# Performance work log

Hardware: AMD Instinct MI355X
Metric: run time of the kernel (lower is better)

The kernel has to match this reference:

```python
import jax, jax.numpy as jnp
import numpy as np

BITS = 4
GROUPSIZE = 128
IN_FEATURES = 4096
OUT_FEATURES = 11008
N_GROUPS = IN_FEATURES // GROUPSIZE  # 32
MASK = (1 << BITS) - 1  # 15


def setup_inputs() -> dict:
    key = jax.random.key(0)
    ks = jax.random.split(key, 5)
    x = jax.random.normal(ks[0], (2, 2048, IN_FEATURES), dtype=jnp.float32)
    qweight = jax.random.randint(ks[1], (IN_FEATURES // 8, OUT_FEATURES), 0, 2**31 - 1, dtype=jnp.int32)
    qzeros = jax.random.randint(ks[2], (N_GROUPS, OUT_FEATURES // 8), 0, 2**31 - 1, dtype=jnp.int32)
    scales = jax.random.uniform(ks[3], (N_GROUPS, OUT_FEATURES), dtype=jnp.float16)
    bias = jax.random.normal(ks[4], (OUT_FEATURES,), dtype=jnp.float32)
    return {"x": x, "qweight": qweight, "qzeros": qzeros, "scales": scales, "bias": bias}


def _dequant(qweight, qzeros, scales):
    # wf = [0, 4, 8, ..., 28]: bit offsets of the 8 int4 nibbles in each int32
    wf = jnp.arange(0, 32, BITS, dtype=jnp.int32)
    # unpack weights: [IN//8, OUT] -> [IN//8, 8, OUT] -> [N_GROUPS, GROUPSIZE, OUT]
    w = (qweight[:, None, :] >> wf[None, :, None]) & MASK
    w = w.reshape(N_GROUPS, GROUPSIZE, OUT_FEATURES).astype(jnp.float32)
    # unpack zeros: [NG, OUT//8] -> [NG, OUT//8, 8] -> [NG, 1, OUT]
    z = (qzeros[:, :, None] >> wf[None, None, :]) & MASK
    z = z.reshape(N_GROUPS, 1, OUT_FEATURES).astype(jnp.float32)
    s = scales.astype(jnp.float32)[:, None, :]  # [NG, 1, OUT]
    # scales * w - scales * z, per group; fused elementwise
    return (s * (w - z)).reshape(IN_FEATURES, OUT_FEATURES)


def reference(x, qweight, qzeros, scales, bias):
    W = _dequant(qweight, qzeros, scales)  # [IN, OUT] fp32
    out = jnp.matmul(x.astype(jnp.float32), W) + bias
    return out
```

## Files before the change

### kernel.cpp

```cpp
#include <hip/hip_runtime.h>
#include <hip/hip_fp16.h>

#define K_DIM 4096
#define N_DIM 11008
#define NZ8   1376
#define BM    256
#define BN    128
#define NT_N  86

typedef _Float16 f16x8 __attribute__((ext_vector_type(8)));
typedef float    f32x4 __attribute__((ext_vector_type(4)));

__global__ __launch_bounds__(256)
void r10_xcvt(const float* __restrict__ x, __half* __restrict__ xh, int nchunks)
{
    int c = blockIdx.x * 256 + threadIdx.x;
    const int stride = gridDim.x * 256;
    for (; c < nchunks; c += stride) {
        const float4 f0 = ((const float4*)x)[2 * c];
        const float4 f1 = ((const float4*)x)[2 * c + 1];
        union { __half2 h2[4]; int4 v; } p;
        p.h2[0] = __floats2half2_rn(f0.x, f1.x);
        p.h2[1] = __floats2half2_rn(f0.y, f1.y);
        p.h2[2] = __floats2half2_rn(f0.z, f1.z);
        p.h2[3] = __floats2half2_rn(f0.w, f1.w);
        ((int4*)xh)[c] = p.v;
    }
}

template<int APATH>
__global__ __launch_bounds__(512, 4)
void r10_gptq_mfma(const float* __restrict__ x,
                   const __half* __restrict__ xh,
                   const int*   __restrict__ qweight,
                   const int*   __restrict__ qzeros,
                   const float* __restrict__ scales,
                   const float* __restrict__ bias,
                   float* __restrict__ out)
{
    __shared__ __align__(16) unsigned char Asm[BM * 64 * 2];
    __shared__ __align__(16) unsigned char Bsm[BN * 64 * 2];

    const int tid  = threadIdx.x;
    const int lane = tid & 63;
    const int wid  = tid >> 6;
    const int wr   = (wid >> 1) * 64;
    const int wc   = (wid & 1) * 64;

    int bid = blockIdx.x;
    const int cpx = gridDim.x >> 3;
    bid = (bid & 7) * cpx + (bid >> 3);
    const int bm0 = (bid / NT_N) * BM;
    const int bn0 = (bid % NT_N) * BN;

    const int arow  = tid >> 1;
    const int ahalf = tid & 1;
    unsigned char* aw = Asm + arow * 128;
    const int asw = (arow & 7) << 4;

    const int bnn  = tid & 127;
    const int bk8q = tid >> 7;
    const int ngl  = bn0 + bnn;
    const int* qwp = qweight + (size_t)bk8q * N_DIM + ngl;
    unsigned char* bw = Bsm + bnn * 128;
    const int bsw = bnn & 7;

    const unsigned mu = 0xE400E400u;
    const __half2 m1024 = *(const __half2*)&mu;

    const int frow = lane & 15;
    const int kb8  = lane >> 4;
    const int fsw  = frow & 7;

    f32x4 acc[4][4];
#pragma unroll
    for (int m = 0; m < 4; ++m)
#pragma unroll
        for (int n = 0; n < 4; ++n)
            acc[m][n] = (f32x4){0.f, 0.f, 0.f, 0.f};

    __half2 scp = __half2{}, nzp = __half2{};

    for (int kt = 0; kt < K_DIM / 64; ++kt) {
        const int k0 = kt * 64;

        if ((k0 & 127) == 0) {
            const int g = k0 >> 7;
            const float sc = scales[(size_t)g * N_DIM + ngl];
            const unsigned zq = (unsigned)qzeros[(size_t)g * NZ8 + (ngl >> 3)];
            const float zf = (float)((zq >> ((ngl & 7) * 4)) & 15u);
            const __half sh = __float2half_rn(sc);
            const __half nh = __float2half_rn(-sc * zf);
            scp = __half2(sh, sh);
            nzp = __half2(nh, nh);
        }

        if constexpr (APATH == 0) {
            const __half* src = xh + (size_t)(bm0 + arow) * K_DIM + k0 + ahalf * 32;
#pragma unroll
            for (int i = 0; i < 4; ++i) {
                const f16x8 v = *(const f16x8*)(src + i * 8);
                *(f16x8*)(aw + ((((ahalf * 4 + i) << 4) ^ asw))) = v;
            }
        } else {
            const float* src = x + (size_t)(bm0 + arow) * K_DIM + k0 + ahalf * 32;
#pragma unroll
            for (int c = 0; c < 4; ++c) {
                const float4 f0 = *(const float4*)(src + c * 8);
                const float4 f1 = *(const float4*)(src + c * 8 + 4);
                union { __half2 h2[4]; f16x8 v; } p;
                p.h2[0] = __floats2half2_rn(f0.x, f1.x);
                p.h2[1] = __floats2half2_rn(f0.y, f1.y);
                p.h2[2] = __floats2half2_rn(f0.z, f1.z);
                p.h2[3] = __floats2half2_rn(f0.w, f1.w);
                *(f16x8*)(aw + ((((ahalf * 4 + c) << 4) ^ asw))) = p.v;
            }
        }

#pragma unroll
        for (int i = 0; i < 2; ++i) {
            const int r = bk8q + 4 * i;
            const unsigned q = (unsigned)qwp[(size_t)(kt * 8 + 4 * i) * N_DIM];
            union { __half2 h2[4]; f16x8 v; } p;
#pragma unroll
            for (int d = 0; d < 4; ++d) {
                unsigned t = ((q >> (4 * d)) & 0x000F000Fu) | 0x64006400u;
                const __half2 th = *(const __half2*)&t;
                p.h2[d] = __hfma2(__hadd2(th, m1024), scp, nzp);
            }
            *(f16x8*)(bw + ((r ^ bsw) << 4)) = p.v;
        }

        __syncthreads();

#pragma unroll
        for (int kh = 0; kh < 2; ++kh) {
            const int ksl = (kh << 2) + kb8;
            f16x8 af[4], bfr[4];
#pragma unroll
            for (int m = 0; m < 4; ++m) {
                const int row = wr + m * 16 + frow;
                af[m] = *(const f16x8*)(Asm + row * 128 + (((ksl ^ fsw) << 4)));
            }
#pragma unroll
            for (int n = 0; n < 4; ++n) {
                const int nn = wc + n * 16 + frow;
                bfr[n] = *(const f16x8*)(Bsm + nn * 128 + (((ksl ^ fsw) << 4)));
            }
#pragma unroll
            for (int m = 0; m < 4; ++m)
#pragma unroll
                for (int n = 0; n < 4; ++n)
                    acc[m][n] = __builtin_amdgcn_mfma_f32_16x16x32_f16(
                        af[m], bfr[n], acc[m][n], 0, 0, 0);
        }

        __syncthreads();
    }

    const int crow0 = (lane >> 4) << 2;
    const int ccol  = lane & 15;
#pragma unroll
    for (int n = 0; n < 4; ++n) {
        const int col = bn0 + wc + n * 16 + ccol;
        const float bv = bias[col];
#pragma unroll
        for (int m = 0; m < 4; ++m) {
            const int row = bm0 + wr + m * 16 + crow0;
#pragma unroll
            for (int j = 0; j < 4; ++j)
                out[(size_t)(row + j) * N_DIM + col] = acc[m][n][j] + bv;
        }
    }
}

extern "C" void kernel_launch(void* const* d_in, const int* in_sizes, int n_in,
                              void* d_out, int out_size, void* d_ws, size_t ws_size,
                              hipStream_t stream)
{
    const float* x   = (const float*)d_in[0];
    const int*   qw  = (const int*)d_in[1];
    const int*   qz  = (const int*)d_in[2];
    const float* scl = (const float*)d_in[3];
    const float* bs  = (const float*)d_in[4];
    float* out = (float*)d_out;

    const int M = in_sizes[0] / K_DIM;
    const size_t xh_bytes = (size_t)M * K_DIM * 2;
    dim3 grid((M / BM) * NT_N);

    if (ws_size >= xh_bytes) {
        __half* xh = (__half*)d_ws;
        const int nchunks = M * K_DIM / 8;
        hipLaunchKernelGGL(r10_xcvt, dim3(2048), dim3(256), 0, stream, x, xh, nchunks);
        hipLaunchKernelGGL((r10_gptq_mfma<0>), grid, dim3(512), 0, stream,
                           x, xh, qw, qz, scl, bs, out);
    } else {
        hipLaunchKernelGGL((r10_gptq_mfma<1>), grid, dim3(512), 0, stream,
                           x, (const __half*)nullptr, qw, qz, scl, bs, out);
    }
}
```

Baseline: 414.2 us.

## Double-buffer LDS with pre-tiled A loaded via global_load_lds, enlarge tile to 256x256

```diff
diff --git a/kernel.cpp b/kernel.cpp
--- a/kernel.cpp
+++ b/kernel.cpp
@@ -5,20 +5,45 @@
 #define N_DIM 11008
 #define NZ8   1376
 #define BM    256
-#define BN    128
-#define NT_N  86
+#define BN    256
+#define BK    64
+#define NT_N  43
+#define NKT   64
+#define ATB   32768
 
 typedef _Float16 f16x8 __attribute__((ext_vector_type(8)));
 typedef float    f32x4 __attribute__((ext_vector_type(4)));
 
+__device__ __forceinline__ f16x8 dq8(unsigned q, __half2 scp, __half2 nzp)
+{
+    const unsigned mu = 0xE400E400u;
+    const __half2 m1024 = *(const __half2*)&mu;
+    union { __half2 h2[4]; f16x8 v; } p;
+#pragma unroll
+    for (int d = 0; d < 4; ++d) {
+        unsigned t = ((q >> (4 * d)) & 0x000F000Fu) | 0x64006400u;
+        p.h2[d] = __hfma2(__hadd2(*(const __half2*)&t, m1024), scp, nzp);
+    }
+    return p.v;
+}
+
 __global__ __launch_bounds__(256)
-void r10_xcvt(const float* __restrict__ x, __half* __restrict__ xh, int nchunks)
+void r11_xcvt(const float* __restrict__ x, __half* __restrict__ xh, int nchunks)
 {
     int c = blockIdx.x * 256 + threadIdx.x;
     const int stride = gridDim.x * 256;
     for (; c < nchunks; c += stride) {
-        const float4 f0 = ((const float4*)x)[2 * c];
-        const float4 f1 = ((const float4*)x)[2 * c + 1];
+        const int w    = c & 2047;
+        const int tidx = c >> 11;
+        const int row  = w >> 3;
+        const int s    = w & 7;
+        const int ls   = s ^ (row & 7);
+        const int mt   = tidx >> 6;
+        const int kt   = tidx & 63;
+        const size_t gm = (size_t)mt * 256 + row;
+        const int kb   = kt * 64 + ls * 8;
+        const float4 f0 = *(const float4*)(x + gm * K_DIM + kb);
+        const float4 f1 = *(const float4*)(x + gm * K_DIM + kb + 4);
         union { __half2 h2[4]; int4 v; } p;
         p.h2[0] = __floats2half2_rn(f0.x, f1.x);
         p.h2[1] = __floats2half2_rn(f0.y, f1.y);
@@ -28,24 +53,43 @@
     }
 }
 
+__device__ __forceinline__ void stage_a_cvt(const float* __restrict__ x,
+                                            unsigned char* __restrict__ abuf,
+                                            int bm0, int kt, int arow, int ahalf, int asw)
+{
+    const float* src = x + (size_t)(bm0 + arow) * K_DIM + kt * 64 + ahalf * 32;
+    unsigned char* aw = abuf + arow * 128;
+#pragma unroll
+    for (int c = 0; c < 4; ++c) {
+        const float4 f0 = *(const float4*)(src + c * 8);
+        const float4 f1 = *(const float4*)(src + c * 8 + 4);
+        union { __half2 h2[4]; f16x8 v; } p;
+        p.h2[0] = __floats2half2_rn(f0.x, f1.x);
+        p.h2[1] = __floats2half2_rn(f0.y, f1.y);
+        p.h2[2] = __floats2half2_rn(f0.z, f1.z);
+        p.h2[3] = __floats2half2_rn(f0.w, f1.w);
+        *(f16x8*)(aw + ((((ahalf * 4 + c) << 4) ^ asw))) = p.v;
+    }
+}
+
 template<int APATH>
-__global__ __launch_bounds__(512, 4)
-void r10_gptq_mfma(const float* __restrict__ x,
-                   const __half* __restrict__ xh,
-                   const int*   __restrict__ qweight,
-                   const int*   __restrict__ qzeros,
-                   const float* __restrict__ scales,
-                   const float* __restrict__ bias,
-                   float* __restrict__ out)
-{
-    __shared__ __align__(16) unsigned char Asm[BM * 64 * 2];
-    __shared__ __align__(16) unsigned char Bsm[BN * 64 * 2];
+__global__ __launch_bounds__(512, 2)
+void r11_gemm(const float* __restrict__ x,
+              const __half* __restrict__ xh,
+              const int*   __restrict__ qweight,
+              const int*   __restrict__ qzeros,
+              const float* __restrict__ scales,
+              const float* __restrict__ bias,
+              float* __restrict__ out)
+{
+    __shared__ __align__(16) unsigned char Asm[2][ATB];
+    __shared__ __align__(16) unsigned char Bsm[2][ATB];
 
     const int tid  = threadIdx.x;
     const int lane = tid & 63;
     const int wid  = tid >> 6;
-    const int wr   = (wid >> 1) * 64;
-    const int wc   = (wid & 1) * 64;
+    const int wr   = (wid >> 2) * 128;
+    const int wc   = (wid & 3) * 64;
 
     int bid = blockIdx.x;
     const int cpx = gridDim.x >> 3;
@@ -53,119 +97,118 @@
     const int bm0 = (bid / NT_N) * BM;
     const int bn0 = (bid % NT_N) * BN;
 
-    const int arow  = tid >> 1;
-    const int ahalf = tid & 1;
-    unsigned char* aw = Asm + arow * 128;
-    const int asw = (arow & 7) << 4;
-
-    const int bnn  = tid & 127;
-    const int bk8q = tid >> 7;
-    const int ngl  = bn0 + bnn;
-    const int* qwp = qweight + (size_t)bk8q * N_DIM + ngl;
-    unsigned char* bw = Bsm + bnn * 128;
+    const int bnn = tid & 255;
+    const int bq  = tid >> 8;
+    const int ngl = bn0 + bnn;
+    const int* qwp = qweight + (size_t)bq * N_DIM + ngl;
     const int bsw = bnn & 7;
 
-    const unsigned mu = 0xE400E400u;
-    const __half2 m1024 = *(const __half2*)&mu;
-
-    const int frow = lane & 15;
-    const int kb8  = lane >> 4;
-    const int fsw  = frow & 7;
-
-    f32x4 acc[4][4];
-#pragma unroll
-    for (int m = 0; m < 4; ++m)
+    const char* agp = (const char*)xh + ((size_t)(bm0 >> 8) * NKT) * ATB + tid * 16;
+
+    const int arow = tid >> 1, ahalf = tid & 1;
+    const int asw  = (arow & 7) << 4;
+
+    const int frow = lane & 15, kb8 = lane >> 4, fsw = frow & 7;
+
+    f32x4 acc[8][4];
+#pragma unroll
+    for (int m = 0; m < 8; ++m)
 #pragma unroll
         for (int n = 0; n < 4; ++n)
             acc[m][n] = (f32x4){0.f, 0.f, 0.f, 0.f};
 
-    __half2 scp = __half2{}, nzp = __half2{};
-
-    for (int kt = 0; kt < K_DIM / 64; ++kt) {
-        const int k0 = kt * 64;
-
-        if ((k0 & 127) == 0) {
-            const int g = k0 >> 7;
-            const float sc = scales[(size_t)g * N_DIM + ngl];
-            const unsigned zq = (unsigned)qzeros[(size_t)g * NZ8 + (ngl >> 3)];
-            const float zf = (float)((zq >> ((ngl & 7) * 4)) & 15u);
-            const __half sh = __float2half_rn(sc);
-            const __half nh = __float2half_rn(-sc * zf);
-            scp = __half2(sh, sh);
-            nzp = __half2(nh, nh);
-        }
-
-        if constexpr (APATH == 0) {
-            const __half* src = xh + (size_t)(bm0 + arow) * K_DIM + k0 + ahalf * 32;
-#pragma unroll
-            for (int i = 0; i < 4; ++i) {
-                const f16x8 v = *(const f16x8*)(src + i * 8);
-                *(f16x8*)(aw + ((((ahalf * 4 + i) << 4) ^ asw))) = v;
-            }
-        } else {
-            const float* src = x + (size_t)(bm0 + arow) * K_DIM + k0 + ahalf * 32;
-#pragma unroll
-            for (int c = 0; c < 4; ++c) {
-                const float4 f0 = *(const float4*)(src + c * 8);
-                const float4 f1 = *(const float4*)(src + c * 8 + 4);
-                union { __half2 h2[4]; f16x8 v; } p;
-                p.h2[0] = __floats2half2_rn(f0.x, f1.x);
-                p.h2[1] = __floats2half2_rn(f0.y, f1.y);
-                p.h2[2] = __floats2half2_rn(f0.z, f1.z);
-                p.h2[3] = __floats2half2_rn(f0.w, f1.w);
-                *(f16x8*)(aw + ((((ahalf * 4 + c) << 4) ^ asw))) = p.v;
-            }
-        }
-
-#pragma unroll
-        for (int i = 0; i < 2; ++i) {
-            const int r = bk8q + 4 * i;
-            const unsigned q = (unsigned)qwp[(size_t)(kt * 8 + 4 * i) * N_DIM];
-            union { __half2 h2[4]; f16x8 v; } p;
-#pragma unroll
-            for (int d = 0; d < 4; ++d) {
-                unsigned t = ((q >> (4 * d)) & 0x000F000Fu) | 0x64006400u;
-                const __half2 th = *(const __half2*)&t;
-                p.h2[d] = __hfma2(__hadd2(th, m1024), scp, nzp);
-            }
-            *(f16x8*)(bw + ((r ^ bsw) << 4)) = p.v;
-        }
-
-        __syncthreads();
+    __half2 scp, nzp;
+    {
+        const float sc = scales[ngl];
+        const unsigned zq = (unsigned)qzeros[ngl >> 3];
+        const float zf = (float)((zq >> ((ngl & 7) * 4)) & 15u);
+        const __half sh = __float2half_rn(sc), nh = __float2half_rn(-sc * zf);
+        scp = __half2(sh, sh); nzp = __half2(nh, nh);
+    }
+
+    if constexpr (APATH == 0) {
+#pragma unroll
+        for (int i = 0; i < 4; ++i)
+            __builtin_amdgcn_global_load_lds((const unsigned int*)(agp + i * 8192),
+                                             (unsigned int*)&Asm[0][tid * 16 + i * 8192],
+                                             16, 0, 0);
+    } else {
+        stage_a_cvt(x, &Asm[0][0], bm0, 0, arow, ahalf, asw);
+    }
+    {
+        unsigned q[4];
+#pragma unroll
+        for (int i = 0; i < 4; ++i) q[i] = (unsigned)qwp[(size_t)(2 * i) * N_DIM];
+#pragma unroll
+        for (int i = 0; i < 4; ++i)
+            *(f16x8*)(&Bsm[0][bnn * 128 + (((bq + 2 * i) ^ bsw) << 4)]) = dq8(q[i], scp, nzp);
+    }
+    __syncthreads();
+
+    for (int kt = 0; kt < NKT; ++kt) {
+        const int cur = kt & 1, nxt = cur ^ 1;
+        unsigned qn[4];
+        const bool hn = (kt + 1 < NKT);
+
+        if (hn) {
+            if constexpr (APATH == 0) {
+                const char* ag = agp + (size_t)(kt + 1) * ATB;
+#pragma unroll
+                for (int i = 0; i < 4; ++i)
+                    __builtin_amdgcn_global_load_lds((const unsigned int*)(ag + i * 8192),
+                                                     (unsigned int*)&Asm[nxt][tid * 16 + i * 8192],
+                                                     16, 0, 0);
+            }
+#pragma unroll
+            for (int i = 0; i < 4; ++i)
+                qn[i] = (unsigned)qwp[(size_t)((kt + 1) * 8 + 2 * i) * N_DIM];
+            if (((kt + 1) & 1) == 0) {
+                const int g = (kt + 1) >> 1;
+                const float sc = scales[(size_t)g * N_DIM + ngl];
+                const unsigned zq = (unsigned)qzeros[(size_t)g * NZ8 + (ngl >> 3)];
+                const float zf = (float)((zq >> ((ngl & 7) * 4)) & 15u);
+                const __half sh = __float2half_rn(sc), nh = __float2half_rn(-sc * zf);
+                scp = __half2(sh, sh); nzp = __half2(nh, nh);
+            }
+        }
 
 #pragma unroll
         for (int kh = 0; kh < 2; ++kh) {
             const int ksl = (kh << 2) + kb8;
-            f16x8 af[4], bfr[4];
-#pragma unroll
-            for (int m = 0; m < 4; ++m) {
-                const int row = wr + m * 16 + frow;
-                af[m] = *(const f16x8*)(Asm + row * 128 + (((ksl ^ fsw) << 4)));
-            }
+            f16x8 bfr[4];
 #pragma unroll
             for (int n = 0; n < 4; ++n) {
                 const int nn = wc + n * 16 + frow;
-                bfr[n] = *(const f16x8*)(Bsm + nn * 128 + (((ksl ^ fsw) << 4)));
-            }
-#pragma unroll
-            for (int m = 0; m < 4; ++m)
+                bfr[n] = *(const f16x8*)(&Bsm[cur][nn * 128 + (((ksl ^ fsw) << 4))]);
+            }
+#pragma unroll
+            for (int m = 0; m < 8; ++m) {
+                const int row = wr + m * 16 + frow;
+                const f16x8 af = *(const f16x8*)(&Asm[cur][row * 128 + (((ksl ^ fsw) << 4))]);
 #pragma unroll
                 for (int n = 0; n < 4; ++n)
                     acc[m][n] = __builtin_amdgcn_mfma_f32_16x16x32_f16(
-                        af[m], bfr[n], acc[m][n], 0, 0, 0);
-        }
-
+                        af, bfr[n], acc[m][n], 0, 0, 0);
+            }
+        }
+
+        if (hn) {
+            if constexpr (APATH == 1)
+                stage_a_cvt(x, &Asm[nxt][0], bm0, kt + 1, arow, ahalf, asw);
+#pragma unroll
+            for (int i = 0; i < 4; ++i)
+                *(f16x8*)(&Bsm[nxt][bnn * 128 + (((bq + 2 * i) ^ bsw) << 4)]) = dq8(qn[i], scp, nzp);
+        }
         __syncthreads();
     }
 
-    const int crow0 = (lane >> 4) << 2;
-    const int ccol  = lane & 15;
+    const int crow0 = (lane >> 4) << 2, ccol = lane & 15;
 #pragma unroll
     for (int n = 0; n < 4; ++n) {
         const int col = bn0 + wc + n * 16 + ccol;
         const float bv = bias[col];
 #pragma unroll
-        for (int m = 0; m < 4; ++m) {
+        for (int m = 0; m < 8; ++m) {
             const int row = bm0 + wr + m * 16 + crow0;
 #pragma unroll
             for (int j = 0; j < 4; ++j)
@@ -192,11 +235,11 @@
     if (ws_size >= xh_bytes) {
         __half* xh = (__half*)d_ws;
         const int nchunks = M * K_DIM / 8;
-        hipLaunchKernelGGL(r10_xcvt, dim3(2048), dim3(256), 0, stream, x, xh, nchunks);
-        hipLaunchKernelGGL((r10_gptq_mfma<0>), grid, dim3(512), 0, stream,
+        hipLaunchKernelGGL(r11_xcvt, dim3(2048), dim3(256), 0, stream, x, xh, nchunks);
+        hipLaunchKernelGGL((r11_gemm<0>), grid, dim3(512), 0, stream,
                            x, xh, qw, qz, scl, bs, out);
     } else {
-        hipLaunchKernelGGL((r10_gptq_mfma<1>), grid, dim3(512), 0, stream,
+        hipLaunchKernelGGL((r11_gemm<1>), grid, dim3(512), 0, stream,
                            x, (const __half*)nullptr, qw, qz, scl, bs, out);
     }
 }
```

Measured after the change: 407.2 us. Within noise of the previous version (-1.7%).
